# Kernel optimization log

Measured on AMD Instinct MI355X. Metric: run time of the kernel, lower is better.

The kernel has to match this reference:

```python
import jax, jax.numpy as jnp
import numpy as np

MAX_DISP = 4  # PWC-Net correlation: displacements in [-4,4] -> 9x9 = 81 channels


def setup_inputs() -> dict:
    key = jax.random.key(0)
    k1, k2 = jax.random.split(key)
    B, C, H, W = 8, 128, 112, 192
    tensorFirst = jax.random.normal(k1, (B, C, H, W), dtype=jnp.float32)
    tensorSecond = jax.random.normal(k2, (B, C, H, W), dtype=jnp.float32)
    return {"tensorFirst": tensorFirst, "tensorSecond": tensorSecond}


def reference(tensorFirst, tensorSecond):
    B, C, H, W = tensorFirst.shape
    D = MAX_DISP
    # zero-pad second by max displacement on each spatial side (rbot padding of 8 = 2*4)
    padded = jnp.pad(tensorSecond, ((0, 0), (0, 0), (D, D), (D, D)))
    outs = []
    # fixed 9x9 displacement grid; channel index = (dy+4)*9 + (dx+4)
    for dy in range(2 * D + 1):
        for dx in range(2 * D + 1):
            shifted = jax.lax.dynamic_slice(padded, (0, 0, dy, dx), (B, C, H, W))
            # dot product over channels, normalized by C (sumelems in the cupy kernel)
            outs.append(jnp.mean(tensorFirst * shifted, axis=1))
    return jnp.stack(outs, axis=1)  # [B, 81, H, W]
```

## Files before the change

kernel.cpp:

```cpp
#include <hip/hip_runtime.h>


namespace {
constexpr int kC = 128;
constexpr int kH = 112;
constexpr int kW = 192;
constexpr int kD = 4;
constexpr int kKD = 9;
constexpr int kHW = kH * kW;
constexpr long long kCHW = (long long)kC * kHW;

constexpr int PX = 4;
constexpr int XG = kW / PX;
constexpr int YT = 4;
constexpr int NT = XG * YT;
constexpr int DYM = 3;
constexpr int NACC = DYM * kKD;

constexpr int SROWF = 200;
constexpr int SROWS = YT + 2;
constexpr int SSLOT = SROWS * 50;
constexpr int STILEF = SROWS * SROWF;
}

__device__ __attribute__((aligned(16))) float g_zero_row[kW] = {};

typedef const __attribute__((address_space(1))) void* gas_ptr;
typedef __attribute__((address_space(3))) void* las_ptr;

__device__ __forceinline__ void gload16(const float* g, float* l) {
  __builtin_amdgcn_global_load_lds((gas_ptr)g, (las_ptr)l, 16, 0, 0);
}

__global__ __launch_bounds__(NT, 3)
void corr81_kernel(const float* __restrict__ first,
                   const float* __restrict__ second,
                   float* __restrict__ out) {
  __shared__ __align__(16) float Sb[2][STILEF];

  const int g = blockIdx.x;
  const int b = g & 7;
  const int i = g >> 3;
  const int dyb = (i % DYM) * DYM;
  const int y0 = (i / DYM) * YT;

  const int tid = threadIdx.x;
  const int xg = tid % XG;
  const int yl = tid / XG;
  const int px0 = xg * PX;

  const float* ssrc[2];
  long long sstr[2];
#pragma unroll
  for (int j = 0; j < 2; ++j) {
    const int slot = j * NT + tid;
    const int r = slot / 50;
    const int k = slot % 50;
    const int ys = y0 + dyb - kD + r;
    const bool ok = (k >= 1) && (k <= 48) && ((unsigned)ys < (unsigned)kH) &&
                    (slot < SSLOT);
    ssrc[j] = ok ? (second + (long long)b * kCHW + (long long)ys * kW +
                    (4 * k - 4))
                 : g_zero_row;
    sstr[j] = ok ? (long long)kHW : 0ll;
  }

  const float* fpg = first + (long long)b * kCHW +
                     (long long)(y0 + yl) * kW + px0;

  float acc[PX][NACC];
#pragma unroll
  for (int p = 0; p < PX; ++p)
#pragma unroll
    for (int a = 0; a < NACC; ++a) acc[p][a] = 0.0f;

  auto stage = [&](int P) {
    gload16(ssrc[0], &Sb[P][tid * 4]);
    if (tid < SSLOT - NT) gload16(ssrc[1], &Sb[P][(tid + NT) * 4]);
    ssrc[0] += sstr[0];
    ssrc[1] += sstr[1];
  };

  auto compute = [&](int P, const float4 f) {
    const float* s = &Sb[P][yl * SROWF + px0];
    const float fv[PX] = {f.x, f.y, f.z, f.w};
#pragma unroll
    for (int j = 0; j < DYM; ++j) {
      const float4 w0 = *(const float4*)(s + j * SROWF);
      const float4 w1 = *(const float4*)(s + j * SROWF + 4);
      const float4 w2 = *(const float4*)(s + j * SROWF + 8);
      const float sw[12] = {w0.x, w0.y, w0.z, w0.w, w1.x, w1.y, w1.z, w1.w,
                            w2.x, w2.y, w2.z, w2.w};
#pragma unroll
      for (int p = 0; p < PX; ++p)
#pragma unroll
        for (int d = 0; d < kKD; ++d)
          acc[p][j * kKD + d] = fmaf(fv[p], sw[p + d], acc[p][j * kKD + d]);
    }
  };

  float4 fa, fb;
  stage(0);
  fa = *(const float4*)fpg; fpg += kHW;
  __syncthreads();
  for (int c = 0; c < kC; c += 2) {
    stage(1);
    fb = *(const float4*)fpg; fpg += kHW;
    compute(0, fa);
    __syncthreads();
    if (c + 2 < kC) {
      stage(0);
      fa = *(const float4*)fpg; fpg += kHW;
    }
    compute(1, fb);
    __syncthreads();
  }

  const float scale = 1.0f / (float)kC;
  float* obase = out + (long long)b * 81 * kHW +
                 (long long)(y0 + yl) * kW + px0;
#pragma unroll
  for (int j = 0; j < DYM; ++j)
#pragma unroll
    for (int d = 0; d < kKD; ++d) {
      float4 o = make_float4(acc[0][j * kKD + d] * scale,
                             acc[1][j * kKD + d] * scale,
                             acc[2][j * kKD + d] * scale,
                             acc[3][j * kKD + d] * scale);
      *(float4*)(obase + (long long)((dyb + j) * kKD + d) * kHW) = o;
    }
}

extern "C" void kernel_launch(void* const* d_in, const int* in_sizes, int n_in,
                              void* d_out, int out_size, void* d_ws, size_t ws_size,
                              hipStream_t stream) {
  const float* first = (const float*)d_in[0];
  const float* second = (const float*)d_in[1];
  float* out = (float*)d_out;

  const int grid = 8 * (kH / YT) * DYM;
  corr81_kernel<<<grid, NT, 0, stream>>>(first, second, out);
}
```

Baseline: 301.2 us.

## Retile correlation: one dy per block, split width into halves, taller row tile

Restructures the work split so each block handles a single vertical displacement over a 96-wide, 8-row tile, instead of three displacements over the full width and 4 rows. This shrinks accumulators from 108 to 36 registers per thread and raises the occupancy target, meant to improve latency hiding. The cost is that the first tensor is reloaded once per dy (9x instead of 3x), and the second tensor's halo columns are re-fetched for each width half, which adds memory traffic.

```diff
diff --git a/kernel.cpp b/kernel.cpp
--- a/kernel.cpp
+++ b/kernel.cpp
@@ -11,16 +11,16 @@
 constexpr long long kCHW = (long long)kC * kHW;
 
 constexpr int PX = 4;
-constexpr int XG = kW / PX;
-constexpr int YT = 4;
+constexpr int XB = 96;
+constexpr int XG = XB / PX;
+constexpr int YT = 8;
 constexpr int NT = XG * YT;
-constexpr int DYM = 3;
-constexpr int NACC = DYM * kKD;
+constexpr int NXT = kW / XB;
 
-constexpr int SROWF = 200;
-constexpr int SROWS = YT + 2;
-constexpr int SSLOT = SROWS * 50;
-constexpr int STILEF = SROWS * SROWF;
+constexpr int SROWF = XB + 8;
+constexpr int SLOTR = SROWF / 4;
+constexpr int SSLOT = YT * SLOTR;
+constexpr int STILEF = YT * SROWF;
 }
 
 __device__ __attribute__((aligned(16))) float g_zero_row[kW] = {};
@@ -32,7 +32,7 @@
   __builtin_amdgcn_global_load_lds((gas_ptr)g, (las_ptr)l, 16, 0, 0);
 }
 
-__global__ __launch_bounds__(NT, 3)
+__global__ __launch_bounds__(NT, 6)
 void corr81_kernel(const float* __restrict__ first,
                    const float* __restrict__ second,
                    float* __restrict__ out) {
@@ -41,38 +41,40 @@
   const int g = blockIdx.x;
   const int b = g & 7;
   const int i = g >> 3;
-  const int dyb = (i % DYM) * DYM;
-  const int y0 = (i / DYM) * YT;
+  const int dy = i % kKD;
+  const int xt = (i / kKD) % NXT;
+  const int y0 = (i / (kKD * NXT)) * YT;
+  const int x0 = xt * XB;
 
   const int tid = threadIdx.x;
   const int xg = tid % XG;
   const int yl = tid / XG;
-  const int px0 = xg * PX;
+  const int px = x0 + xg * PX;
 
   const float* ssrc[2];
   long long sstr[2];
 #pragma unroll
   for (int j = 0; j < 2; ++j) {
-    const int slot = j * NT + tid;
-    const int r = slot / 50;
-    const int k = slot % 50;
-    const int ys = y0 + dyb - kD + r;
-    const bool ok = (k >= 1) && (k <= 48) && ((unsigned)ys < (unsigned)kH) &&
-                    (slot < SSLOT);
-    ssrc[j] = ok ? (second + (long long)b * kCHW + (long long)ys * kW +
-                    (4 * k - 4))
+    const int s = j * NT + tid;
+    const int r = s / SLOTR;
+    const int k = s % SLOTR;
+    const int gc = x0 - 4 + 4 * k;
+    const int ys = y0 + dy - kD + r;
+    const bool ok = (s < SSLOT) && (gc >= 0) && (gc <= kW - 4) &&
+                    ((unsigned)ys < (unsigned)kH);
+    ssrc[j] = ok ? (second + (long long)b * kCHW + (long long)ys * kW + gc)
                  : g_zero_row;
     sstr[j] = ok ? (long long)kHW : 0ll;
   }
 
   const float* fpg = first + (long long)b * kCHW +
-                     (long long)(y0 + yl) * kW + px0;
+                     (long long)(y0 + yl) * kW + px;
 
-  float acc[PX][NACC];
+  float acc[PX][kKD];
 #pragma unroll
   for (int p = 0; p < PX; ++p)
 #pragma unroll
-    for (int a = 0; a < NACC; ++a) acc[p][a] = 0.0f;
+    for (int d = 0; d < kKD; ++d) acc[p][d] = 0.0f;
 
   auto stage = [&](int P) {
     gload16(ssrc[0], &Sb[P][tid * 4]);
@@ -82,21 +84,18 @@
   };
 
   auto compute = [&](int P, const float4 f) {
-    const float* s = &Sb[P][yl * SROWF + px0];
+    const float* s = &Sb[P][yl * SROWF + xg * PX];
+    const float4 w0 = *(const float4*)(s);
+    const float4 w1 = *(const float4*)(s + 4);
+    const float4 w2 = *(const float4*)(s + 8);
+    const float sw[12] = {w0.x, w0.y, w0.z, w0.w, w1.x, w1.y, w1.z, w1.w,
+                          w2.x, w2.y, w2.z, w2.w};
     const float fv[PX] = {f.x, f.y, f.z, f.w};
 #pragma unroll
-    for (int j = 0; j < DYM; ++j) {
-      const float4 w0 = *(const float4*)(s + j * SROWF);
-      const float4 w1 = *(const float4*)(s + j * SROWF + 4);
-      const float4 w2 = *(const float4*)(s + j * SROWF + 8);
-      const float sw[12] = {w0.x, w0.y, w0.z, w0.w, w1.x, w1.y, w1.z, w1.w,
-                            w2.x, w2.y, w2.z, w2.w};
+    for (int p = 0; p < PX; ++p)
 #pragma unroll
-      for (int p = 0; p < PX; ++p)
-#pragma unroll
-        for (int d = 0; d < kKD; ++d)
-          acc[p][j * kKD + d] = fmaf(fv[p], sw[p + d], acc[p][j * kKD + d]);
-    }
+      for (int d = 0; d < kKD; ++d)
+        acc[p][d] = fmaf(fv[p], sw[p + d], acc[p][d]);
   };
 
   float4 fa, fb;
@@ -117,18 +116,14 @@
   }
 
   const float scale = 1.0f / (float)kC;
-  float* obase = out + (long long)b * 81 * kHW +
-                 (long long)(y0 + yl) * kW + px0;
+  float* obase = out + ((long long)b * 81 + (long long)dy * kKD) * kHW +
+                 (long long)(y0 + yl) * kW + px;
 #pragma unroll
-  for (int j = 0; j < DYM; ++j)
-#pragma unroll
-    for (int d = 0; d < kKD; ++d) {
-      float4 o = make_float4(acc[0][j * kKD + d] * scale,
-                             acc[1][j * kKD + d] * scale,
-                             acc[2][j * kKD + d] * scale,
-                             acc[3][j * kKD + d] * scale);
-      *(float4*)(obase + (long long)((dyb + j) * kKD + d) * kHW) = o;
-    }
+  for (int d = 0; d < kKD; ++d) {
+    float4 o = make_float4(acc[0][d] * scale, acc[1][d] * scale,
+                           acc[2][d] * scale, acc[3][d] * scale);
+    *(float4*)(obase + (long long)d * kHW) = o;
+  }
 }
 
 extern "C" void kernel_launch(void* const* d_in, const int* in_sizes, int n_in,
@@ -138,6 +133,6 @@
   const float* second = (const float*)d_in[1];
   float* out = (float*)d_out;
 
-  const int grid = 8 * (kH / YT) * DYM;
+  const int grid = 8 * (kH / YT) * NXT * kKD;
   corr81_kernel<<<grid, NT, 0, stream>>>(first, second, out);
 }
```

Measured after the change: 292.5 us. -2.9%, faster.
